# Kernel optimization log

Measured on AMD Instinct MI355X. Metric: run time of the kernel, lower is better.

## Reference

```python
import jax, jax.numpy as jnp
import numpy as np

B, T, K, H = 32, 128, 16, 4   # batch, agents, in_dim, num_heads
A = 2                          # out_dim (action dim)
H1 = H2 = 256
LOG_STD_MIN, LOG_STD_MAX = -20.0, 2.0


def _linear_params(key, out_dim, in_dim, uniform_w=None):
    k1, k2 = jax.random.split(key)
    if uniform_w is not None:
        w = jax.random.uniform(k1, (out_dim, in_dim), minval=-uniform_w, maxval=uniform_w)
        b = jax.random.uniform(k2, (out_dim,), minval=-uniform_w, maxval=uniform_w)
    else:
        bound = 1.0 / np.sqrt(in_dim)
        w = jax.random.uniform(k1, (out_dim, in_dim), minval=-bound, maxval=bound)
        b = jax.random.uniform(k2, (out_dim,), minval=-bound, maxval=bound)
    return w.astype(jnp.float32), b.astype(jnp.float32)


def setup_inputs() -> dict:
    key = jax.random.key(0)
    ks = jax.random.split(key, 10)
    state = jax.random.normal(ks[0], (B, T, K), dtype=jnp.float32)
    eps = jax.random.normal(ks[1], (B, T, A), dtype=jnp.float32)
    Wq, bq = _linear_params(ks[2], K * H, K)
    Wk, bk = _linear_params(ks[3], K * H, K)
    Wv, bv = _linear_params(ks[4], K * H, K)
    W1, b1 = _linear_params(ks[5], H1, K * H + K)
    W2, b2 = _linear_params(ks[6], H2, H1)
    Wmu, bmu = _linear_params(ks[7], A, H2, uniform_w=0.003)
    Wls, bls = _linear_params(ks[8], A, H2, uniform_w=0.003)
    return {"state": state, "eps": eps, "Wq": Wq, "bq": bq, "Wk": Wk, "bk": bk,
            "Wv": Wv, "bv": bv, "W1": W1, "b1": b1, "W2": W2, "b2": b2,
            "Wmu": Wmu, "bmu": bmu, "Wls": Wls, "bls": bls}


def reference(state, eps, Wq, bq, Wk, bk, Wv, bv, W1, b1, W2, b2, Wmu, bmu, Wls, bls):
    b, t, k = state.shape
    h = H
    # rel[b,i,j] = state[b,j] - state[b,i]
    rel = state[:, None, :, :] - state[:, :, None, :]          # (b,t,t,k)
    q = jax.nn.relu(state @ Wq.T + bq).reshape(b, t, h, k)     # (b,t,h,k)
    q = q.transpose(0, 2, 1, 3)                                # (b,h,t,k)
    Kt = jax.nn.relu(rel @ Wk.T + bk).reshape(b, t, t, h, k)   # (b,i,j,h,k)
    V = jax.nn.relu(rel @ Wv.T + bv).reshape(b, t, t, h, k)
    # scores over pairwise keys vs per-agent query; softmax over j (dim=2 in torch)
    s = jnp.einsum('bijhk,bhik->bhij', Kt, q) / jnp.sqrt(jnp.float32(k))
    w = jax.nn.softmax(s, axis=3)                              # softmax over j
    x = jnp.einsum('bhij,bijhk->bhik', w, V)                   # (b,h,t,k)
    x = x.transpose(0, 2, 1, 3).reshape(b, t, h * k)           # (b,t,h*k)
    x = jnp.concatenate([x, state], axis=-1)                   # (b,t,h*k+k)
    x = jax.nn.relu(x @ W1.T + b1)
    x = jax.nn.relu(x @ W2.T + b2)
    mu = jnp.tanh(x @ Wmu.T + bmu)
    log_std = jnp.tanh(x @ Wls.T + bls)
    log_std = LOG_STD_MIN + 0.5 * (LOG_STD_MAX - LOG_STD_MIN) * (log_std + 1.0)
    std = jnp.exp(log_std)
    z = mu + std * eps                                         # rsample
    action = jnp.tanh(z)
    # Normal log_prob with (z-mu)/std == eps, minus tanh correction
    log_prob = (-0.5 * eps * eps - log_std - 0.5 * jnp.log(2.0 * jnp.pi)) \
               - jnp.log(1.0 - action * action + 1e-7)
    log_prob = jnp.sum(log_prob, axis=-1, keepdims=True)
    return action, log_prob
```

## Files before the change

### kernel.cpp

```cpp
#include <hip/hip_runtime.h>
#include <math.h>

#define NB 32
#define NT 128
#define KD 16

#define QG_OFF   0u
#define PKF_OFF  1048576u
#define PVT_OFF  3145728u
#define W1P_OFF  3670016u
#define W2P_OFF  3719168u

typedef float f32x4 __attribute__((ext_vector_type(4)));
typedef short bf16x8 __attribute__((ext_vector_type(8)));
typedef __fp16 f16x2 __attribute__((ext_vector_type(2)));
union U4B8 { uint4 u; bf16x8 h; };
union U4H8 { uint4 u; f16x2 h[4]; };

#define L_PK 0
#define L_PV 34816
#define L_P  52224
#define L_TOT 69632
#define L_X  0
#define L_H1 3584
#define L_H2 12032

__device__ __forceinline__ unsigned short bf16rne(float f) {
    unsigned u = __float_as_uint(f);
    return (unsigned short)((u + 0x7fffu + ((u >> 16) & 1u)) >> 16);
}
__device__ __forceinline__ void unpack8(uint4 u, float* f) {
    f[0] = __uint_as_float(u.x << 16); f[1] = __uint_as_float(u.x & 0xffff0000u);
    f[2] = __uint_as_float(u.y << 16); f[3] = __uint_as_float(u.y & 0xffff0000u);
    f[4] = __uint_as_float(u.z << 16); f[5] = __uint_as_float(u.z & 0xffff0000u);
    f[6] = __uint_as_float(u.w << 16); f[7] = __uint_as_float(u.w & 0xffff0000u);
}
__device__ __forceinline__ f16x2 pkmax(f16x2 a, f16x2 b) {
    f16x2 d;
    asm("v_pk_max_f16 %0, %1, %2" : "=v"(d) : "v"(a), "v"(b));
    return d;
}
#if __has_builtin(__builtin_amdgcn_fdot2)
#define FDOT2(a, b, c) __builtin_amdgcn_fdot2((a), (b), (c), false)
#else
#define FDOT2(a, b, c) ((c) + (float)(a)[0] * (float)(b)[0] + (float)(a)[1] * (float)(b)[1])
#endif

__global__ __launch_bounds__(256) void prep_kernel(
    const float* __restrict__ state,
    const float* __restrict__ Wq, const float* __restrict__ bq,
    const float* __restrict__ Wk, const float* __restrict__ Wv,
    const float* __restrict__ W1, const float* __restrict__ W2,
    char* __restrict__ wsb)
{
    const int blk = blockIdx.x, tid = threadIdx.x;
    float* Qg  = (float*)(wsb + QG_OFF);
    float* PkF = (float*)(wsb + PKF_OFF);
    unsigned short* PvT = (unsigned short*)(wsb + PVT_OFF);

    if (blk < 128) {
        __shared__ float Wl[3][64][17];
        __shared__ float Sl[32][17];
        const int b = blk >> 2, r0 = (blk & 3) * 32;
        for (int idx = tid; idx < 1024; idx += 256) {
            int o = idx >> 4, m = idx & 15;
            Wl[0][o][m] = Wq[idx];
            Wl[1][o][m] = Wk[idx];
            Wl[2][o][m] = Wv[idx];
        }
        for (int idx = tid; idx < 512; idx += 256)
            Sl[idx >> 4][idx & 15] = state[(size_t)(b * NT + r0) * KD + idx];
        __syncthreads();
        const int o = tid & 63, rr = tid >> 6;
        float wqv[16], wkv[16], wvv[16];
        #pragma unroll
        for (int m = 0; m < 16; ++m) {
            wqv[m] = Wl[0][o][m]; wkv[m] = Wl[1][o][m]; wvv[m] = Wl[2][o][m];
        }
        const float bqo = bq[o];
        for (int r = rr; r < 32; r += 4) {
            float aq = bqo, ak = 0.f, av = 0.f;
            #pragma unroll
            for (int m = 0; m < 16; ++m) {
                float s = Sl[r][m];
                aq = fmaf(s, wqv[m], aq);
                ak = fmaf(s, wkv[m], ak);
                av = fmaf(s, wvv[m], av);
            }
            int row = b * NT + r0 + r;
            Qg[row * 64 + o]  = fmaxf(aq, 0.f) * 0.25f;
            PkF[row * 64 + o] = ak;
            __fp16 hv = (__fp16)av;
            PvT[b * 8192 + o * NT + (r0 + r)] = *(unsigned short*)&hv;
        }
    } else if (blk < 140) {
        int fi = (blk - 128) * 256 + tid;
        int l = fi & 63, rest = fi >> 6;
        int t = rest & 15, ks = rest >> 4;
        int n = t * 16 + (l & 15);
        int kb = ks * 32 + (l >> 4) * 8;
        unsigned short v[8];
        #pragma unroll
        for (int j = 0; j < 8; ++j) {
            int k = kb + j;
            v[j] = (k < 80) ? bf16rne(W1[n * 80 + k]) : (unsigned short)0;
        }
        uint4 u;
        u.x = (unsigned)v[0] | ((unsigned)v[1] << 16);
        u.y = (unsigned)v[2] | ((unsigned)v[3] << 16);
        u.z = (unsigned)v[4] | ((unsigned)v[5] << 16);
        u.w = (unsigned)v[6] | ((unsigned)v[7] << 16);
        ((uint4*)(wsb + W1P_OFF))[fi] = u;
    } else {
        int fi = (blk - 140) * 256 + tid;
        int l = fi & 63, rest = fi >> 6;
        int t = rest & 15, ks = rest >> 4;
        int n = t * 16 + (l & 15);
        int kb = ks * 32 + (l >> 4) * 8;
        unsigned short v[8];
        #pragma unroll
        for (int j = 0; j < 8; ++j) v[j] = bf16rne(W2[n * 256 + kb + j]);
        uint4 u;
        u.x = (unsigned)v[0] | ((unsigned)v[1] << 16);
        u.y = (unsigned)v[2] | ((unsigned)v[3] << 16);
        u.z = (unsigned)v[4] | ((unsigned)v[5] << 16);
        u.w = (unsigned)v[6] | ((unsigned)v[7] << 16);
        ((uint4*)(wsb + W2P_OFF))[fi] = u;
    }
}

__global__ __launch_bounds__(1024, 4) void actor_kernel(
    const float* __restrict__ state, const float* __restrict__ eps,
    const float* __restrict__ bkg, const float* __restrict__ bvg,
    const float* __restrict__ b1g, const float* __restrict__ b2g,
    const float* __restrict__ Wmu, const float* __restrict__ bmu,
    const float* __restrict__ Wls, const float* __restrict__ bls,
    const char* __restrict__ wsb, float* __restrict__ out)
{
    __shared__ __align__(16) char sm[L_TOT];
    float* smPk = (float*)(sm + L_PK);

    const int tid = threadIdx.x, w = tid >> 6, lane = tid & 63;
    const int bid = blockIdx.x;
    const int b = (bid & 7) * 4 + ((bid >> 3) & 3);
    const int tile = bid >> 5;
    const int iloc = tile * 16 + w;
    const int row  = b * NT + iloc;
    const int h = lane >> 4, s = lane & 15, h16 = h << 4;
    const int g = h, lr = s;
    const int n1 = w * 16 + lr;

    const float* Qg  = (const float*)(wsb + QG_OFF);
    const float* PkF = (const float*)(wsb + PKF_OFF);

    float qA[16], bkr[16];
    {
        const float4* qa  = (const float4*)(Qg + (size_t)row * 64 + h16);
        const float4* bk4 = (const float4*)(bkg + h16);
        #pragma unroll
        for (int q4 = 0; q4 < 4; ++q4) {
            float4 a = qa[q4], k4 = bk4[q4];
            qA[q4*4+0]=a.x; qA[q4*4+1]=a.y; qA[q4*4+2]=a.z; qA[q4*4+3]=a.w;
            bkr[q4*4+0]=k4.x; bkr[q4*4+1]=k4.y; bkr[q4*4+2]=k4.z; bkr[q4*4+3]=k4.w;
        }
    }
    const float bvo = bvg[lane];
    float stt = 0.f;
    if (tid < 256)
        stt = state[((size_t)b * NT + tile * 16 + (tid >> 4)) * KD + (tid & 15)];

    {
        const uint4* srcK = (const uint4*)(PkF + (size_t)b * NT * 64);
        #pragma unroll
        for (int it = 0; it < 2; ++it) {
            int idx = tid + it * 1024;
            int r = idx >> 4, c = idx & 15;
            *(uint4*)(smPk + r * 68 + c * 4) = srcK[idx];
        }
        const uint4* srcV = (const uint4*)(wsb + PVT_OFF) + (size_t)b * 1024;
        {
            int o = tid >> 4, c = tid & 15;
            *(uint4*)(sm + L_PV + o * 272 + c * 16) = srcV[tid];
        }
    }
    __syncthreads();

    float mbeff[16], dotc = 0.f;
    {
        const float* pkI = smPk + iloc * 68 + h16;
        #pragma unroll
        for (int k = 0; k < 16; ++k) {
            float pk = pkI[k];
            mbeff[k] = pk - bkr[k];
            dotc = fmaf(qA[k], bkr[k] - pk, dotc);
        }
    }

    float sc[8];
    #pragma unroll
    for (int jj = 0; jj < 8; ++jj) {
        const float4* pk = (const float4*)(smPk + (s + (jj << 4)) * 68 + h16);
        float a = dotc;
        #pragma unroll
        for (int q4 = 0; q4 < 4; ++q4) {
            float4 v = pk[q4];
            float f[4] = {v.x, v.y, v.z, v.w};
            #pragma unroll
            for (int kk = 0; kk < 4; ++kk) {
                int k = q4 * 4 + kk;
                a = fmaf(qA[k], fmaxf(f[kk], mbeff[k]), a);
            }
        }
        sc[jj] = a;
    }

    float mx = sc[0];
    #pragma unroll
    for (int jj = 1; jj < 8; ++jj) mx = fmaxf(mx, sc[jj]);
    #pragma unroll
    for (int off = 1; off < 16; off <<= 1) mx = fmaxf(mx, __shfl_xor(mx, off));
    float l = 0.f;
    #pragma unroll
    for (int jj = 0; jj < 8; ++jj) { sc[jj] = __expf(sc[jj] - mx); l += sc[jj]; }
    #pragma unroll
    for (int off = 1; off < 16; off <<= 1) l += __shfl_xor(l, off);
    const float rl = 1.0f / l;
    {
        __fp16* prow = (__fp16*)(sm + L_P) + (w * 4 + h) * 136;
        #pragma unroll
        for (int jj = 0; jj < 8; ++jj) prow[(jj << 4) + s] = (__fp16)sc[jj];
    }
    asm volatile("s_waitcnt lgkmcnt(0)" ::: "memory");
    __builtin_amdgcn_sched_barrier(0);

    float xA;
    {
        const __fp16 pvi = *((const __fp16*)(sm + L_PV) + lane * 136 + iloc);
        const float mbvf = (float)pvi - bvo;
        const __fp16 mbvh = (__fp16)mbvf;
        const f16x2 mbv2 = {mbvh, mbvh};
        const uint4* vrow = (const uint4*)(sm + L_PV + lane * 272);
        const uint4* prow = (const uint4*)(sm + L_P + (w * 4 + h) * 272);
        float acc = 0.f;
        #pragma unroll
        for (int u = 0; u < 16; ++u) {
            U4H8 v; v.u = vrow[u];
            U4H8 p; p.u = prow[u];
            #pragma unroll
            for (int t = 0; t < 4; ++t)
                acc = FDOT2(p.h[t], pkmax(v.h[t], mbv2), acc);
        }
        xA = fmaf(rl, acc, -(float)mbvh);
    }
    __syncthreads();

    ((unsigned short*)(sm + L_X))[w * 104 + lane] = bf16rne(xA);
    if (tid < 256) {
        unsigned short* xr = (unsigned short*)(sm + L_X) + (tid >> 4) * 104;
        xr[64 + (tid & 15)] = bf16rne(stt);
        xr[80 + (tid & 15)] = 0;
    }
    __syncthreads();

    const uint4* W1P = (const uint4*)(wsb + W1P_OFF);
    const uint4* W2P = (const uint4*)(wsb + W2P_OFF);

    {
        f32x4 a1 = {0.f, 0.f, 0.f, 0.f};
        #pragma unroll
        for (int ks = 0; ks < 3; ++ks) {
            U4B8 av; av.u = *(const uint4*)(sm + L_X + (lr * 104 + ks * 32 + g * 8) * 2);
            U4B8 bw; bw.u = W1P[((ks << 4) + w) * 64 + lane];
            a1 = __builtin_amdgcn_mfma_f32_16x16x32_bf16(av.h, bw.h, a1, 0, 0, 0);
        }
        const float bn = b1g[n1];
        #pragma unroll
        for (int qq = 0; qq < 4; ++qq)
            *((unsigned short*)(sm + L_H1) + (4 * g + qq) * 264 + n1) =
                bf16rne(fmaxf(a1[qq] + bn, 0.f));
    }
    __syncthreads();

    {
        f32x4 a2 = {0.f, 0.f, 0.f, 0.f};
        #pragma unroll
        for (int ks = 0; ks < 8; ++ks) {
            U4B8 av; av.u = *(const uint4*)(sm + L_H1 + (lr * 264 + ks * 32 + g * 8) * 2);
            U4B8 bw; bw.u = W2P[((ks << 4) + w) * 64 + lane];
            a2 = __builtin_amdgcn_mfma_f32_16x16x32_bf16(av.h, bw.h, a2, 0, 0, 0);
        }
        const float bn = b2g[n1];
        #pragma unroll
        for (int qq = 0; qq < 4; ++qq)
            *((unsigned short*)(sm + L_H2) + (4 * g + qq) * 264 + n1) =
                bf16rne(fmaxf(a2[qq] + bn, 0.f));
    }
    __syncthreads();

    if (tid < 256) {
        const int m = tid >> 4, cc = tid & 15;
        float hbuf[16];
        uint4 ha = *(const uint4*)(sm + L_H2 + (m * 264 + cc * 16) * 2);
        uint4 hb = *(const uint4*)(sm + L_H2 + (m * 264 + cc * 16 + 8) * 2);
        unpack8(ha, hbuf); unpack8(hb, hbuf + 8);
        float d0 = 0.f, d1 = 0.f, d2 = 0.f, d3 = 0.f;
        #pragma unroll
        for (int kk = 0; kk < 16; ++kk) {
            int k = cc * 16 + kk;
            float hv = hbuf[kk];
            d0 = fmaf(hv, Wmu[k], d0);
            d1 = fmaf(hv, Wmu[256 + k], d1);
            d2 = fmaf(hv, Wls[k], d2);
            d3 = fmaf(hv, Wls[256 + k], d3);
        }
        #pragma unroll
        for (int off = 1; off < 16; off <<= 1) {
            d0 += __shfl_xor(d0, off);
            d1 += __shfl_xor(d1, off);
            d2 += __shfl_xor(d2, off);
            d3 += __shfl_xor(d3, off);
        }
        if (cc == 0) {
            const int orow = b * NT + tile * 16 + m;
            float mu0 = tanhf(d0 + bmu[0]);
            float mu1 = tanhf(d1 + bmu[1]);
            float t2  = tanhf(d2 + bls[0]);
            float t3  = tanhf(d3 + bls[1]);
            float ls0 = -20.f + 11.f * (t2 + 1.f);
            float ls1 = -20.f + 11.f * (t3 + 1.f);
            float e0 = eps[orow * 2], e1 = eps[orow * 2 + 1];
            float z0 = mu0 + __expf(ls0) * e0;
            float z1 = mu1 + __expf(ls1) * e1;
            float a0 = tanhf(z0), a1 = tanhf(z1);
            out[orow * 2]     = a0;
            out[orow * 2 + 1] = a1;
            float lp = -0.5f * e0 * e0 - ls0 - 0.91893853320467274f - __logf(1.f - a0 * a0 + 1e-7f)
                     + -0.5f * e1 * e1 - ls1 - 0.91893853320467274f - __logf(1.f - a1 * a1 + 1e-7f);
            out[NB * NT * 2 + orow] = lp;
        }
    }
}

extern "C" void kernel_launch(void* const* d_in, const int* in_sizes, int n_in,
                              void* d_out, int out_size, void* d_ws, size_t ws_size,
                              hipStream_t stream) {
    const float* state = (const float*)d_in[0];
    const float* eps   = (const float*)d_in[1];
    const float* Wq    = (const float*)d_in[2];
    const float* bq    = (const float*)d_in[3];
    const float* Wk    = (const float*)d_in[4];
    const float* bk    = (const float*)d_in[5];
    const float* Wv    = (const float*)d_in[6];
    const float* bv    = (const float*)d_in[7];
    const float* W1    = (const float*)d_in[8];
    const float* b1    = (const float*)d_in[9];
    const float* W2    = (const float*)d_in[10];
    const float* b2    = (const float*)d_in[11];
    const float* Wmu   = (const float*)d_in[12];
    const float* bmu   = (const float*)d_in[13];
    const float* Wls   = (const float*)d_in[14];
    const float* bls   = (const float*)d_in[15];
    float* out = (float*)d_out;
    char* wsb  = (char*)d_ws;

    prep_kernel<<<172, 256, 0, stream>>>(state, Wq, bq, Wk, Wv, W1, W2, wsb);
    actor_kernel<<<256, 1024, 0, stream>>>(state, eps, bk, bv, b1, b2,
                                           Wmu, bmu, Wls, bls, wsb, out);
}
```

Measured before the change: 23.44 us.

## Split actor work into 512 blocks of 8 agents with two MFMA tiles per wave

Halves the block size from 1024 to 512 threads and doubles the grid, so each block handles 8 query agents instead of 16. Each wave now computes two 16-column output tiles in the MLP layers, with padding rows zeroed for the 16-row MFMA. The output head is spread over all threads, one dot product per (row, output), and a small final stage writes the results. The aim is to use more CUs and cut shared-memory use per block, at the cost of staging per-batch K/V twice as often and wasting half of each MFMA on padding rows.

```diff
diff --git a/kernel.cpp b/kernel.cpp
--- a/kernel.cpp
+++ b/kernel.cpp
@@ -20,7 +20,7 @@
 #define L_PK 0
 #define L_PV 34816
 #define L_P  52224
-#define L_TOT 69632
+#define L_TOT 60928
 #define L_X  0
 #define L_H1 3584
 #define L_H2 12032
@@ -129,7 +129,7 @@
     }
 }
 
-__global__ __launch_bounds__(1024, 4) void actor_kernel(
+__global__ __launch_bounds__(512, 4) void actor_kernel(
     const float* __restrict__ state, const float* __restrict__ eps,
     const float* __restrict__ bkg, const float* __restrict__ bvg,
     const float* __restrict__ b1g, const float* __restrict__ b2g,
@@ -142,13 +142,14 @@
 
     const int tid = threadIdx.x, w = tid >> 6, lane = tid & 63;
     const int bid = blockIdx.x;
-    const int b = (bid & 7) * 4 + ((bid >> 3) & 3);
-    const int tile = bid >> 5;
-    const int iloc = tile * 16 + w;
+    const int b    = (bid & 7) * 4 + ((bid >> 3) >> 4);
+    const int tile = (bid >> 3) & 15;
+    const int iloc = tile * 8 + w;
     const int row  = b * NT + iloc;
     const int h = lane >> 4, s = lane & 15, h16 = h << 4;
     const int g = h, lr = s;
-    const int n1 = w * 16 + lr;
+    const int t0 = 2 * w;
+    const int n0 = w * 32 + lr, n1 = n0 + 16;
 
     const float* Qg  = (const float*)(wsb + QG_OFF);
     const float* PkF = (const float*)(wsb + PKF_OFF);
@@ -166,21 +167,23 @@
     }
     const float bvo = bvg[lane];
     float stt = 0.f;
-    if (tid < 256)
-        stt = state[((size_t)b * NT + tile * 16 + (tid >> 4)) * KD + (tid & 15)];
+    if (tid < 128)
+        stt = state[((size_t)b * NT + tile * 8 + (tid >> 4)) * KD + (tid & 15)];
 
     {
         const uint4* srcK = (const uint4*)(PkF + (size_t)b * NT * 64);
         #pragma unroll
-        for (int it = 0; it < 2; ++it) {
-            int idx = tid + it * 1024;
+        for (int it = 0; it < 4; ++it) {
+            int idx = tid + it * 512;
             int r = idx >> 4, c = idx & 15;
             *(uint4*)(smPk + r * 68 + c * 4) = srcK[idx];
         }
         const uint4* srcV = (const uint4*)(wsb + PVT_OFF) + (size_t)b * 1024;
-        {
-            int o = tid >> 4, c = tid & 15;
-            *(uint4*)(sm + L_PV + o * 272 + c * 16) = srcV[tid];
+        #pragma unroll
+        for (int it = 0; it < 2; ++it) {
+            int idx = tid + it * 512;
+            int o = idx >> 4, c = idx & 15;
+            *(uint4*)(sm + L_PV + o * 272 + c * 16) = srcV[idx];
         }
     }
     __syncthreads();
@@ -255,89 +258,99 @@
     __syncthreads();
 
     ((unsigned short*)(sm + L_X))[w * 104 + lane] = bf16rne(xA);
-    if (tid < 256) {
+    if (tid < 128) {
         unsigned short* xr = (unsigned short*)(sm + L_X) + (tid >> 4) * 104;
         xr[64 + (tid & 15)] = bf16rne(stt);
         xr[80 + (tid & 15)] = 0;
     }
+    if (tid < 384) {
+        int r = 8 + tid / 48, c2 = (tid % 48) * 2;
+        *(unsigned*)((unsigned short*)(sm + L_X) + r * 104 + c2) = 0u;
+    }
     __syncthreads();
 
     const uint4* W1P = (const uint4*)(wsb + W1P_OFF);
     const uint4* W2P = (const uint4*)(wsb + W2P_OFF);
 
     {
-        f32x4 a1 = {0.f, 0.f, 0.f, 0.f};
+        f32x4 a0 = {0.f, 0.f, 0.f, 0.f}, a1 = a0;
         #pragma unroll
         for (int ks = 0; ks < 3; ++ks) {
             U4B8 av; av.u = *(const uint4*)(sm + L_X + (lr * 104 + ks * 32 + g * 8) * 2);
-            U4B8 bw; bw.u = W1P[((ks << 4) + w) * 64 + lane];
-            a1 = __builtin_amdgcn_mfma_f32_16x16x32_bf16(av.h, bw.h, a1, 0, 0, 0);
-        }
-        const float bn = b1g[n1];
-        #pragma unroll
-        for (int qq = 0; qq < 4; ++qq)
+            U4B8 b0; b0.u = W1P[((ks << 4) + t0) * 64 + lane];
+            U4B8 b1; b1.u = W1P[((ks << 4) + t0 + 1) * 64 + lane];
+            a0 = __builtin_amdgcn_mfma_f32_16x16x32_bf16(av.h, b0.h, a0, 0, 0, 0);
+            a1 = __builtin_amdgcn_mfma_f32_16x16x32_bf16(av.h, b1.h, a1, 0, 0, 0);
+        }
+        const float bn0 = b1g[n0], bn1 = b1g[n1];
+        #pragma unroll
+        for (int qq = 0; qq < 4; ++qq) {
+            *((unsigned short*)(sm + L_H1) + (4 * g + qq) * 264 + n0) =
+                bf16rne(fmaxf(a0[qq] + bn0, 0.f));
             *((unsigned short*)(sm + L_H1) + (4 * g + qq) * 264 + n1) =
-                bf16rne(fmaxf(a1[qq] + bn, 0.f));
-    }
-    __syncthreads();
-
-    {
-        f32x4 a2 = {0.f, 0.f, 0.f, 0.f};
+                bf16rne(fmaxf(a1[qq] + bn1, 0.f));
+        }
+    }
+    __syncthreads();
+
+    {
+        f32x4 a0 = {0.f, 0.f, 0.f, 0.f}, a1 = a0;
         #pragma unroll
         for (int ks = 0; ks < 8; ++ks) {
             U4B8 av; av.u = *(const uint4*)(sm + L_H1 + (lr * 264 + ks * 32 + g * 8) * 2);
-            U4B8 bw; bw.u = W2P[((ks << 4) + w) * 64 + lane];
-            a2 = __builtin_amdgcn_mfma_f32_16x16x32_bf16(av.h, bw.h, a2, 0, 0, 0);
-        }
-        const float bn = b2g[n1];
-        #pragma unroll
-        for (int qq = 0; qq < 4; ++qq)
+            U4B8 b0; b0.u = W2P[((ks << 4) + t0) * 64 + lane];
+            U4B8 b1; b1.u = W2P[((ks << 4) + t0 + 1) * 64 + lane];
+            a0 = __builtin_amdgcn_mfma_f32_16x16x32_bf16(av.h, b0.h, a0, 0, 0, 0);
+            a1 = __builtin_amdgcn_mfma_f32_16x16x32_bf16(av.h, b1.h, a1, 0, 0, 0);
+        }
+        const float bn0 = b2g[n0], bn1 = b2g[n1];
+        #pragma unroll
+        for (int qq = 0; qq < 4; ++qq) {
+            *((unsigned short*)(sm + L_H2) + (4 * g + qq) * 264 + n0) =
+                bf16rne(fmaxf(a0[qq] + bn0, 0.f));
             *((unsigned short*)(sm + L_H2) + (4 * g + qq) * 264 + n1) =
-                bf16rne(fmaxf(a2[qq] + bn, 0.f));
-    }
-    __syncthreads();
-
-    if (tid < 256) {
-        const int m = tid >> 4, cc = tid & 15;
+                bf16rne(fmaxf(a1[qq] + bn1, 0.f));
+        }
+    }
+    __syncthreads();
+
+    {
+        const int g2 = tid >> 4, m = g2 >> 2, d = g2 & 3, cc = tid & 15;
+        const float* wrow = (d < 2) ? (Wmu + d * 256) : (Wls + (d - 2) * 256);
         float hbuf[16];
         uint4 ha = *(const uint4*)(sm + L_H2 + (m * 264 + cc * 16) * 2);
         uint4 hb = *(const uint4*)(sm + L_H2 + (m * 264 + cc * 16 + 8) * 2);
         unpack8(ha, hbuf); unpack8(hb, hbuf + 8);
-        float d0 = 0.f, d1 = 0.f, d2 = 0.f, d3 = 0.f;
-        #pragma unroll
-        for (int kk = 0; kk < 16; ++kk) {
-            int k = cc * 16 + kk;
-            float hv = hbuf[kk];
-            d0 = fmaf(hv, Wmu[k], d0);
-            d1 = fmaf(hv, Wmu[256 + k], d1);
-            d2 = fmaf(hv, Wls[k], d2);
-            d3 = fmaf(hv, Wls[256 + k], d3);
-        }
-        #pragma unroll
-        for (int off = 1; off < 16; off <<= 1) {
-            d0 += __shfl_xor(d0, off);
-            d1 += __shfl_xor(d1, off);
-            d2 += __shfl_xor(d2, off);
-            d3 += __shfl_xor(d3, off);
-        }
+        float dd = 0.f;
+        #pragma unroll
+        for (int kk = 0; kk < 16; ++kk)
+            dd = fmaf(hbuf[kk], wrow[cc * 16 + kk], dd);
+        #pragma unroll
+        for (int off = 1; off < 16; off <<= 1) dd += __shfl_xor(dd, off);
+        float* hd = (float*)(sm + L_P);
         if (cc == 0) {
-            const int orow = b * NT + tile * 16 + m;
-            float mu0 = tanhf(d0 + bmu[0]);
-            float mu1 = tanhf(d1 + bmu[1]);
-            float t2  = tanhf(d2 + bls[0]);
-            float t3  = tanhf(d3 + bls[1]);
-            float ls0 = -20.f + 11.f * (t2 + 1.f);
-            float ls1 = -20.f + 11.f * (t3 + 1.f);
-            float e0 = eps[orow * 2], e1 = eps[orow * 2 + 1];
-            float z0 = mu0 + __expf(ls0) * e0;
-            float z1 = mu1 + __expf(ls1) * e1;
-            float a0 = tanhf(z0), a1 = tanhf(z1);
-            out[orow * 2]     = a0;
-            out[orow * 2 + 1] = a1;
-            float lp = -0.5f * e0 * e0 - ls0 - 0.91893853320467274f - __logf(1.f - a0 * a0 + 1e-7f)
-                     + -0.5f * e1 * e1 - ls1 - 0.91893853320467274f - __logf(1.f - a1 * a1 + 1e-7f);
-            out[NB * NT * 2 + orow] = lp;
-        }
+            float bias = (d < 2) ? bmu[d] : bls[d - 2];
+            hd[m * 4 + d] = tanhf(dd + bias);
+        }
+    }
+    __syncthreads();
+    if (tid < 8) {
+        const float* hd = (const float*)(sm + L_P);
+        const int m = tid;
+        const int orow = b * NT + tile * 8 + m;
+        float lp = 0.f;
+        #pragma unroll
+        for (int d = 0; d < 2; ++d) {
+            float mu  = hd[m * 4 + d];
+            float lsr = hd[m * 4 + 2 + d];
+            float ls  = -20.f + 11.f * (lsr + 1.f);
+            float e   = eps[orow * 2 + d];
+            float z   = mu + __expf(ls) * e;
+            float a   = tanhf(z);
+            out[orow * 2 + d] = a;
+            lp += -0.5f * e * e - ls - 0.91893853320467274f - __logf(1.f - a * a + 1e-7f);
+        }
+        out[NB * NT * 2 + orow] = lp;
     }
 }
 
@@ -364,6 +377,6 @@
     char* wsb  = (char*)d_ws;
 
     prep_kernel<<<172, 256, 0, stream>>>(state, Wq, bq, Wk, Wv, W1, W2, wsb);
-    actor_kernel<<<256, 1024, 0, stream>>>(state, eps, bk, bv, b1, b2,
-                                           Wmu, bmu, Wls, bls, wsb, out);
-}
+    actor_kernel<<<512, 512, 0, stream>>>(state, eps, bk, bv, b1, b2,
+                                          Wmu, bmu, Wls, bls, wsb, out);
+}
```

After: 22.77 us. -2.9%, faster.
